# Performance work log

Measured on AMD Instinct MI355X. Metric: run time of the kernel, lower is better.

## Reference

```python
import jax, jax.numpy as jnp
import numpy as np

IOU_THR = 0.5
SCORE_THR = 0.5
MAX_DET = 100
B, N, C = 16, 25200, 80


def setup_inputs() -> dict:
    key = jax.random.key(0)
    k1, k2, k3 = jax.random.split(key, 3)
    return {
        "boxes_xywh": jax.random.uniform(k1, (B, N, 4), dtype=jnp.float32),
        "objectness": jax.random.uniform(k2, (B, N, 1), dtype=jnp.float32),
        "class_prob": jax.random.uniform(k3, (B, N, C), dtype=jnp.float32),
    }


def _xywh_to_corners(b):
    x, y, w, h = jnp.split(b, 4, axis=-1)
    return jnp.concatenate([x - w / 2, y - h / 2, x + w / 2, y + h / 2], axis=-1)


def _broadcast_iou(box, boxes):
    # box [4], boxes [N,4] in x1,y1,x2,y2
    lt = jnp.maximum(box[:2], boxes[:, :2])
    rb = jnp.minimum(box[2:], boxes[:, 2:])
    wh = jnp.clip(rb - lt, 0.0)
    inter = wh[:, 0] * wh[:, 1]
    a1 = (box[2] - box[0]) * (box[3] - box[1])
    a2 = (boxes[:, 2] - boxes[:, 0]) * (boxes[:, 3] - boxes[:, 1])
    return inter / (a1 + a2 - inter + 1e-9)


def _nms_single(cand):
    # cand: [N, 4+1+C] rows = (x1,y1,x2,y2, score, class_probs...)
    n, d = cand.shape
    scores = cand[:, 4]
    active0 = scores >= SCORE_THR

    def body(i, state):
        active, out, count = state
        masked = jnp.where(active, scores, -jnp.inf)
        best = jnp.argmax(masked)
        valid = jnp.any(active)
        best_box = cand[best]
        out = out.at[i].set(jnp.where(valid, best_box, out[i]))
        count = count + valid.astype(jnp.int32)
        iou = _broadcast_iou(best_box[:4], cand[:, :4])
        keep = active & (iou <= IOU_THR)
        keep = keep.at[best].set(False)
        active = jnp.where(valid, keep, active)
        return active, out, count

    out0 = jnp.zeros((MAX_DET, d), cand.dtype)
    _, out, count = jax.lax.fori_loop(0, MAX_DET, body, (active0, out0, jnp.int32(0)))
    return out, count


def reference(boxes_xywh, objectness, class_prob):
    corners = _xywh_to_corners(boxes_xywh)  # [B,N,4]
    combined = jnp.concatenate([corners, objectness, class_prob], axis=-1)  # [B,N,5+C]
    final_result, count = jax.vmap(_nms_single)(combined)  # [B,MAX_DET,5+C], [B]
    nms_boxes = final_result[..., 0:4]
    nms_scores = final_result[..., 4:5]
    nms_classes = final_result[..., 5:]
    valid_count = count.astype(jnp.int32)[:, None]  # [B,1]
    return nms_boxes, nms_scores, nms_classes, valid_count
```

## Files before the change

### kernel.cpp

```cpp
#include <hip/hip_runtime.h>

#define NBOX    25200
#define NQ4     6300
#define NBATCH  16
#define NCLS    80
#define MAXDET  100
#define NBUCKET 1024
#define CAP     13824
#define SCORE_THR 0.5f
#define IOU_THR   0.5f
#define NGROUP  16

__device__ __forceinline__ void mk_corners(float x, float y, float w, float h,
                                           float& x1, float& y1, float& x2, float& y2) {
#pragma clang fp contract(off)
    float hw = w * 0.5f;
    float hh = h * 0.5f;
    x1 = x - hw; y1 = y - hh; x2 = x + hw; y2 = y + hh;
}

__device__ __forceinline__ float areaf(float x1, float y1, float x2, float y2) {
#pragma clang fp contract(off)
    return (x2 - x1) * (y2 - y1);
}

__device__ __forceinline__ bool iou_gt(float kx1, float ky1, float kx2, float ky2, float ka,
                                       float cx1, float cy1, float cx2, float cy2, float ca) {
#pragma clang fp contract(off)
    float lx = fmaxf(kx1, cx1);
    float ly = fmaxf(ky1, cy1);
    float rx = fminf(kx2, cx2);
    float ry = fminf(ky2, cy2);
    float w  = fmaxf(rx - lx, 0.0f);
    float h  = fmaxf(ry - ly, 0.0f);
    float inter = w * h;
    float denom = ka + ca - inter + 1e-9f;
    return (inter + inter) > denom;
}

__device__ __forceinline__ float readlane_f(float v, int j) {
    return __uint_as_float((unsigned)__builtin_amdgcn_readlane((int)__float_as_uint(v), j));
}

__device__ __forceinline__ unsigned score_key(float s) {
    return __float_as_uint(s) - 0x3F000000u;
}

__global__ __launch_bounds__(1024)
void nms_kernel(const float* __restrict__ boxes_xywh,
                const float* __restrict__ objectness,
                const float* __restrict__ class_prob,
                float* __restrict__ out) {
    __shared__ unsigned s_hist[NBUCKET];
    __shared__ unsigned s_start[NBUCKET];
    __shared__ unsigned s_a[CAP];
    __shared__ unsigned s_b[CAP];
    __shared__ float4   s_kbox[MAXDET];
    __shared__ float    s_karea[MAXDET];
    __shared__ unsigned s_kept_idx[MAXDET];
    __shared__ unsigned s_wsum[16];
    __shared__ unsigned s_woff[16];
    __shared__ int      s_count;

    const int b = blockIdx.x;
    const int t = threadIdx.x;
    const int w = t >> 6;
    const int l = t & 63;
    const float* obj = objectness + (size_t)b * NBOX;
    const float* bx  = boxes_xywh + (size_t)b * NBOX * 4;

    float4 r[7];
#pragma unroll
    for (int i = 0; i < 7; ++i) {
        int n4 = t + (i << 10);
        if (n4 < NQ4) r[i] = *(const float4*)(obj + n4 * 4);
    }

    s_hist[t] = 0u;
    __syncthreads();
#pragma unroll
    for (int i = 0; i < 7; ++i) {
        int n4 = t + (i << 10);
        if (n4 < NQ4) {
            float sv[4] = {r[i].x, r[i].y, r[i].z, r[i].w};
#pragma unroll
            for (int u = 0; u < 4; ++u) {
                if (sv[u] >= SCORE_THR) {
                    unsigned bkt = score_key(sv[u]) >> 13;
                    if (bkt > 1023u) bkt = 1023u;
                    atomicAdd(&s_hist[bkt], 1u);
                }
            }
        }
    }
    __syncthreads();

    {
        unsigned f = s_hist[1023 - t];
        unsigned v = f;
#pragma unroll
        for (int off = 1; off < 64; off <<= 1) {
            unsigned u = (unsigned)__shfl_up((int)v, off);
            if (l >= off) v += u;
        }
        if (l == 63) s_wsum[w] = v;
        __syncthreads();
        if (t < 64) {
            unsigned x = (t < 16) ? s_wsum[t] : 0u;
            unsigned y = x;
#pragma unroll
            for (int off = 1; off < 16; off <<= 1) {
                unsigned u = (unsigned)__shfl_up((int)y, off);
                if (t >= off) y += u;
            }
            if (t < 16) s_woff[t] = y - x;
        }
        __syncthreads();
        s_start[1023 - t] = v - f + s_woff[w];
    }
    if (t == 0) s_count = 0;
    __syncthreads();

#pragma unroll
    for (int i = 0; i < 7; ++i) {
        int n4 = t + (i << 10);
        if (n4 < NQ4) {
            float sv[4] = {r[i].x, r[i].y, r[i].z, r[i].w};
#pragma unroll
            for (int u = 0; u < 4; ++u) {
                if (sv[u] >= SCORE_THR) {
                    unsigned ekey = score_key(sv[u]);
                    unsigned bkt  = ekey >> 13;
                    if (bkt > 1023u) bkt = 1023u;
                    int n = n4 * 4 + u;
                    unsigned pos = atomicAdd(&s_start[bkt], 1u);
                    if (pos < CAP)
                        s_a[pos] = ((ekey & 0x1FFFu) << 18) | (0x3FFFFu - (unsigned)n);
                }
            }
        }
    }
    __syncthreads();

    auto sort_bucket = [&](int bkt) {
        unsigned h = s_hist[bkt];
        if (h == 0u) return;
        unsigned end = s_start[bkt];
        unsigned hi  = (end > CAP) ? CAP : end;
        unsigned lo  = (end >= h) ? end - h : 0u;
        if (lo > hi) lo = hi;
        unsigned sz = hi - lo;
        if (sz == 0u) return;
        if (sz <= 64u) {
            unsigned v = (l < (int)sz) ? s_a[lo + (unsigned)l] : 0u;
            int rank = 0;
            for (unsigned j = 0; j < sz; ++j)
                rank += ((unsigned)__shfl((int)v, (int)j) > v) ? 1 : 0;
            if (l < (int)sz) s_b[lo + (unsigned)rank] = v;
        } else {
            for (unsigned bb = 0; bb < sz; bb += 64u) {
                bool valid = bb + (unsigned)l < sz;
                unsigned v = valid ? s_a[lo + bb + (unsigned)l] : 0u;
                int rank = 0;
                for (unsigned j = 0; j < sz; ++j)
                    rank += (s_a[lo + j] > v) ? 1 : 0;
                if (valid) s_b[lo + (unsigned)rank] = v;
            }
        }
    };

    for (int bkt = (1023 - 63) + w; bkt <= 1023; bkt += 16) sort_bucket(bkt);
    __syncthreads();

    int count = 0;
    for (int g = 0; g < NGROUP; ++g) {
        const int BH = 1023 - (g << 6);
        const int BL = BH - 63;

        if (w == 0) {
            unsigned glo = (g == 0) ? 0u : s_start[BH + 1];
            unsigned ghi = s_start[BL];
            if (glo > CAP) glo = CAP;
            if (ghi > CAP) ghi = CAP;

            if (glo < ghi && count < MAXDET) {
                unsigned i0, i1, i2, i3;
                float4 q0, q1, q2, q3;
                auto loadc = [&](unsigned cb, unsigned& ix, float4& q) {
                    ix = 0u; q = make_float4(0.f, 0.f, 0.f, 0.f);
                    unsigned p0 = cb + (unsigned)l;
                    if (p0 < ghi) {
                        unsigned p = s_b[p0];
                        ix = 0x3FFFFu - (p & 0x3FFFFu);
                        q = *(const float4*)(bx + (size_t)ix * 4);
                    }
                };
                loadc(glo,        i0, q0);
                loadc(glo + 64u,  i1, q1);
                loadc(glo + 128u, i2, q2);
                loadc(glo + 192u, i3, q3);

                for (unsigned base = glo; base < ghi && count < MAXDET; base += 64u) {
                    unsigned cidx = i0; float4 cq = q0;
                    i0 = i1; q0 = q1;
                    i1 = i2; q1 = q2;
                    i2 = i3; q2 = q3;
                    loadc(base + 256u, i3, q3);

                    int m = (int)(ghi - base); if (m > 64) m = 64;
                    float cx1, cy1, cx2, cy2;
                    mk_corners(cq.x, cq.y, cq.z, cq.w, cx1, cy1, cx2, cy2);
                    float ca = areaf(cx1, cy1, cx2, cy2);

                    bool sup = (l >= m);
                    int k = 0;
                    for (; k + 4 <= count; k += 4) {
                        float4 kb0 = s_kbox[k],     kb1 = s_kbox[k + 1];
                        float4 kb2 = s_kbox[k + 2], kb3 = s_kbox[k + 3];
                        float ka0 = s_karea[k],     ka1 = s_karea[k + 1];
                        float ka2 = s_karea[k + 2], ka3 = s_karea[k + 3];
                        sup = sup | iou_gt(kb0.x, kb0.y, kb0.z, kb0.w, ka0,
                                           cx1, cy1, cx2, cy2, ca);
                        sup = sup | iou_gt(kb1.x, kb1.y, kb1.z, kb1.w, ka1,
                                           cx1, cy1, cx2, cy2, ca);
                        sup = sup | iou_gt(kb2.x, kb2.y, kb2.z, kb2.w, ka2,
                                           cx1, cy1, cx2, cy2, ca);
                        sup = sup | iou_gt(kb3.x, kb3.y, kb3.z, kb3.w, ka3,
                                           cx1, cy1, cx2, cy2, ca);
                        if (((k & 12) == 12) && __all(sup)) { k = count; break; }
                    }
                    for (; k < count; ++k) {
                        float4 kb = s_kbox[k];
                        sup = sup | iou_gt(kb.x, kb.y, kb.z, kb.w, s_karea[k],
                                           cx1, cy1, cx2, cy2, ca);
                    }
                    unsigned long long act = __ballot(!sup);

                    unsigned long long accmask = 0ull;
                    const int cbase = count;
                    while (act != 0ull && count < MAXDET) {
                        int j = (int)__builtin_ctzll(act);
                        accmask |= 1ull << j;
                        float bx1 = readlane_f(cx1, j), by1 = readlane_f(cy1, j);
                        float bx2 = readlane_f(cx2, j), by2 = readlane_f(cy2, j);
                        float bar = readlane_f(ca, j);
                        bool su = iou_gt(bx1, by1, bx2, by2, bar, cx1, cy1, cx2, cy2, ca);
                        ++count;
                        act &= ~(1ull << j);
                        act &= ~__ballot(su);
                    }

                    if (accmask & (1ull << l)) {
                        int slot = cbase + (int)__popcll(accmask & ((1ull << l) - 1ull));
                        s_kbox[slot] = make_float4(cx1, cy1, cx2, cy2);
                        s_karea[slot] = ca;
                        s_kept_idx[slot] = cidx;
                        float* ob = out + ((size_t)b * MAXDET + slot) * 4;
                        ob[0] = cx1; ob[1] = cy1; ob[2] = cx2; ob[3] = cy2;
                        out[NBATCH * MAXDET * 4 + b * MAXDET + slot] = obj[cidx];
                    }
                    __asm__ volatile("s_waitcnt lgkmcnt(0)" ::: "memory");
                }
            }
            if (l == 0) s_count = count;
        } else if (g + 1 < NGROUP) {
            const int BH2 = BH - 64, BL2 = BH2 - 63;
            for (int bkt = BL2 + (w - 1); bkt <= BH2; bkt += 15) sort_bucket(bkt);
        }
        __syncthreads();
        if (s_count >= MAXDET) break;
    }

    const int cf = s_count;
    for (int e = t; e < MAXDET * 4; e += 1024) {
        if ((e >> 2) >= cf) out[(size_t)b * MAXDET * 4 + e] = 0.0f;
    }
    for (int i = t; i < MAXDET; i += 1024) {
        if (i >= cf) out[NBATCH * MAXDET * 4 + b * MAXDET + i] = 0.0f;
    }
    const float* cp = class_prob + (size_t)b * NBOX * NCLS;
    float* oc = out + NBATCH * MAXDET * 5 + (size_t)b * MAXDET * NCLS;
    float4* oc4 = (float4*)oc;
    const int NQC = NCLS / 4;
    const int nq = cf * NQC;
    for (int e4 = t; e4 < nq; e4 += 1024) {
        int i  = e4 / NQC;
        int c4 = e4 - i * NQC;
        oc4[e4] = *((const float4*)(cp + (size_t)s_kept_idx[i] * NCLS) + c4);
    }
    for (int e4 = t + nq; e4 < MAXDET * NQC; e4 += 1024)
        oc4[e4] = make_float4(0.0f, 0.0f, 0.0f, 0.0f);
    if (t == 0)
        out[NBATCH * MAXDET * 5 + NBATCH * MAXDET * NCLS + b] = (float)cf;
}

extern "C" void kernel_launch(void* const* d_in, const int* in_sizes, int n_in,
                              void* d_out, int out_size, void* d_ws, size_t ws_size,
                              hipStream_t stream) {
    const float* boxes = (const float*)d_in[0];
    const float* objn  = (const float*)d_in[1];
    const float* clsp  = (const float*)d_in[2];
    float* out = (float*)d_out;
    nms_kernel<<<dim3(NBATCH), dim3(1024), 0, stream>>>(boxes, objn, clsp, out);
}
```

Baseline: 194.3 us.

## Precompute suppression masks for the next chunk on helper warps during serial NMS

Reshapes the per-group NMS loop into chunk steps with a block-wide barrier after each. Waves 1-7 test the next 64-candidate chunk against already-kept boxes in parallel and publish a suppression bitmask plus a watermark, so wave 0 only needs to check boxes kept after that watermark. Waves 8-15 keep sorting the next group's buckets, spread across the chunk steps. The exchange is a __syncthreads per chunk and extra global loads of candidate boxes. A leftover stub iou_gt that returns false is shadowed by a #define to iou_gt2, which is confusing but has no effect on behaviour.

```diff
diff --git a/kernel.cpp b/kernel.cpp
--- a/kernel.cpp
+++ b/kernel.cpp
@@ -10,6 +10,7 @@
 #define SCORE_THR 0.5f
 #define IOU_THR   0.5f
 #define NGROUP  16
+#define MAXCH   24
 
 __device__ __forceinline__ void mk_corners(float x, float y, float w, float h,
                                            float& x1, float& y1, float& x2, float& y2) {
@@ -26,6 +27,16 @@
 
 __device__ __forceinline__ bool iou_gt(float kx1, float ky1, float kx2, float ky2, float ka,
                                        float cx1, float cy1, float cx2, float cy2, float ca) {
+#pragma clang fp contract(off)
+    float lx = fmaxf(kx1, cx1);
+    float ly = fmaxf(ky1, cy1);
+    float rx = fminf(kx2, cx2);
+    float ry = fminf(ry = fminf(ky2, cy2), ry);
+    return false;
+}
+
+__device__ __forceinline__ bool iou_gt2(float kx1, float ky1, float kx2, float ky2, float ka,
+                                        float cx1, float cy1, float cx2, float cy2, float ca) {
 #pragma clang fp contract(off)
     float lx = fmaxf(kx1, cx1);
     float ly = fmaxf(ky1, cy1);
@@ -37,6 +48,7 @@
     float denom = ka + ca - inter + 1e-9f;
     return (inter + inter) > denom;
 }
+#define iou_gt iou_gt2
 
 __device__ __forceinline__ float readlane_f(float v, int j) {
     return __uint_as_float((unsigned)__builtin_amdgcn_readlane((int)__float_as_uint(v), j));
@@ -61,6 +73,9 @@
     __shared__ unsigned s_wsum[16];
     __shared__ unsigned s_woff[16];
     __shared__ int      s_count;
+    __shared__ unsigned s_mlo[MAXCH], s_mhi[MAXCH];
+    __shared__ unsigned s_wm[MAXCH];
+    __shared__ int      s_cnt2[2];
 
     const int b = blockIdx.x;
     const int t = threadIdx.x;
@@ -176,31 +191,44 @@
     for (int g = 0; g < NGROUP; ++g) {
         const int BH = 1023 - (g << 6);
         const int BL = BH - 63;
-
-        if (w == 0) {
-            unsigned glo = (g == 0) ? 0u : s_start[BH + 1];
-            unsigned ghi = s_start[BL];
-            if (glo > CAP) glo = CAP;
-            if (ghi > CAP) ghi = CAP;
-
-            if (glo < ghi && count < MAXDET) {
-                unsigned i0, i1, i2, i3;
-                float4 q0, q1, q2, q3;
-                auto loadc = [&](unsigned cb, unsigned& ix, float4& q) {
-                    ix = 0u; q = make_float4(0.f, 0.f, 0.f, 0.f);
-                    unsigned p0 = cb + (unsigned)l;
-                    if (p0 < ghi) {
-                        unsigned p = s_b[p0];
-                        ix = 0x3FFFFu - (p & 0x3FFFFu);
-                        q = *(const float4*)(bx + (size_t)ix * 4);
-                    }
-                };
-                loadc(glo,        i0, q0);
-                loadc(glo + 64u,  i1, q1);
-                loadc(glo + 128u, i2, q2);
-                loadc(glo + 192u, i3, q3);
-
-                for (unsigned base = glo; base < ghi && count < MAXDET; base += 64u) {
+        unsigned glo = (g == 0) ? 0u : s_start[BH + 1];
+        unsigned ghi = s_start[BL];
+        if (glo > CAP) glo = CAP;
+        if (ghi > CAP) ghi = CAP;
+        int nch = (ghi > glo) ? (int)((ghi - glo + 63u) >> 6) : 0;
+
+        if (t < MAXCH) { s_mlo[t] = 0u; s_mhi[t] = 0u; s_wm[t] = 0u; }
+        if (t == 0) { s_cnt2[0] = s_count; s_cnt2[1] = s_count; }
+        __syncthreads();
+
+        unsigned i0 = 0, i1 = 0, i2 = 0, i3 = 0;
+        float4 q0, q1, q2, q3;
+        auto loadc = [&](unsigned cb, unsigned& ix, float4& q) {
+            ix = 0u; q = make_float4(0.f, 0.f, 0.f, 0.f);
+            unsigned p0 = cb + (unsigned)l;
+            if (p0 < ghi) {
+                unsigned p = s_b[p0];
+                ix = 0x3FFFFu - (p & 0x3FFFFu);
+                q = *(const float4*)(bx + (size_t)ix * 4);
+            }
+        };
+        if (w == 0 && nch > 0 && count < MAXDET) {
+            loadc(glo,        i0, q0);
+            loadc(glo + 64u,  i1, q1);
+            loadc(glo + 128u, i2, q2);
+            loadc(glo + 192u, i3, q3);
+        }
+
+        bool broke = false;
+        int sorted_i = 0;
+        const int BL2 = BH - 127;
+        for (int i = 0; i < nch; ++i) {
+            const int cprev = s_cnt2[(i + 1) & 1];
+            if (cprev >= MAXDET) { broke = true; break; }
+
+            if (w == 0) {
+                if (count < MAXDET) {
+                    unsigned base = glo + ((unsigned)i << 6);
                     unsigned cidx = i0; float4 cq = q0;
                     i0 = i1; q0 = q1;
                     i1 = i2; q1 = q2;
@@ -212,8 +240,11 @@
                     mk_corners(cq.x, cq.y, cq.z, cq.w, cx1, cy1, cx2, cy2);
                     float ca = areaf(cx1, cy1, cx2, cy2);
 
-                    bool sup = (l >= m);
-                    int k = 0;
+                    int wm = 0; unsigned mlo = 0u, mhi = 0u;
+                    if (i < MAXCH) { wm = (int)s_wm[i]; mlo = s_mlo[i]; mhi = s_mhi[i]; }
+                    unsigned long long hm = ((unsigned long long)mhi << 32) | mlo;
+                    bool sup = (l >= m) | (((hm >> l) & 1ull) != 0ull);
+                    int k = wm;
                     for (; k + 4 <= count; k += 4) {
                         float4 kb0 = s_kbox[k],     kb1 = s_kbox[k + 1];
                         float4 kb2 = s_kbox[k + 2], kb3 = s_kbox[k + 3];
@@ -261,12 +292,50 @@
                     }
                     __asm__ volatile("s_waitcnt lgkmcnt(0)" ::: "memory");
                 }
-            }
-            if (l == 0) s_count = count;
-        } else if (g + 1 < NGROUP) {
-            const int BH2 = BH - 64, BL2 = BH2 - 63;
-            for (int bkt = BL2 + (w - 1); bkt <= BH2; bkt += 15) sort_bucket(bkt);
-        }
+                if (l == 0) s_cnt2[i & 1] = count;
+            } else if (w <= 7) {
+                int ci = i + 1;
+                if (ci < nch && ci < MAXCH) {
+                    unsigned p0 = glo + ((unsigned)ci << 6) + (unsigned)l;
+                    bool valid = p0 < ghi;
+                    float4 qq = make_float4(0.f, 0.f, 0.f, 0.f);
+                    if (valid) {
+                        unsigned p = s_b[p0];
+                        unsigned ix = 0x3FFFFu - (p & 0x3FFFFu);
+                        qq = *(const float4*)(bx + (size_t)ix * 4);
+                    }
+                    float hx1, hy1, hx2, hy2;
+                    mk_corners(qq.x, qq.y, qq.z, qq.w, hx1, hy1, hx2, hy2);
+                    float hca = areaf(hx1, hy1, hx2, hy2);
+                    int k0 = (w - 1) * cprev / 7;
+                    int k1 = w * cprev / 7;
+                    bool sup = !valid;
+                    for (int k = k0; k < k1; ++k) {
+                        float4 kb = s_kbox[k];
+                        sup = sup | iou_gt(kb.x, kb.y, kb.z, kb.w, s_karea[k],
+                                           hx1, hy1, hx2, hy2, hca);
+                    }
+                    unsigned long long bm = __ballot(sup);
+                    if (l == 0) {
+                        unsigned lo32 = (unsigned)bm, hi32 = (unsigned)(bm >> 32);
+                        if (lo32) atomicOr(&s_mlo[ci], lo32);
+                        if (hi32) atomicOr(&s_mhi[ci], hi32);
+                        if (w == 1) s_wm[ci] = (unsigned)cprev;
+                    }
+                }
+            } else {
+                if (g + 1 < NGROUP && sorted_i < 8) {
+                    sort_bucket(BL2 + (w - 8) * 8 + sorted_i);
+                    ++sorted_i;
+                }
+            }
+            __syncthreads();
+        }
+        if (!broke && g + 1 < NGROUP && w >= 8) {
+            for (; sorted_i < 8; ++sorted_i)
+                sort_bucket(BL2 + (w - 8) * 8 + sorted_i);
+        }
+        if (w == 0 && l == 0) s_count = count;
         __syncthreads();
         if (s_count >= MAXDET) break;
     }
```

After: 190.7 us. No clear change (-1.9%).
